# Optimization experiments

Measured on AMD Instinct MI355X. Metric: run time of the kernel, lower is better.

Reference implementation:

```python
import jax, jax.numpy as jnp
import numpy as np

N_NODES = 50000
N_EDGES = 800000
D_FEAT = 128
HIDDEN = 128
N_CLASSES = 40


def setup_inputs() -> dict:
    key = jax.random.key(0)
    ks = jax.random.split(key, 8)
    s = 1.0 / np.sqrt(D_FEAT)
    return {
        "x": jax.random.normal(ks[0], (N_NODES, D_FEAT), jnp.float32),
        "edge_index": jax.random.randint(ks[1], (2, N_EDGES), 0, N_NODES, jnp.int64),
        "Wl0": jax.random.normal(ks[2], (D_FEAT, HIDDEN), jnp.float32) * s,
        "bl0": jnp.zeros((HIDDEN,), jnp.float32),
        "Wr0": jax.random.normal(ks[3], (D_FEAT, HIDDEN), jnp.float32) * s,
        "Wl1": jax.random.normal(ks[4], (HIDDEN, HIDDEN), jnp.float32) * s,
        "bl1": jnp.zeros((HIDDEN,), jnp.float32),
        "Wr1": jax.random.normal(ks[5], (HIDDEN, HIDDEN), jnp.float32) * s,
        "Wl2": jax.random.normal(ks[6], (HIDDEN, N_CLASSES), jnp.float32) * s,
        "bl2": jnp.zeros((N_CLASSES,), jnp.float32),
        "Wr2": jax.random.normal(ks[7], (HIDDEN, N_CLASSES), jnp.float32) * s,
    }


def _sage_conv(x, src, dst, Wl, bl, Wr):
    # PyG SAGEConv (mean aggr): out = lin_l(mean_{j in N(i)} x_j) + lin_r(x_i)
    msg_sum = jax.ops.segment_sum(x[src], dst, num_segments=N_NODES)  # [N, d]
    deg = jax.ops.segment_sum(jnp.ones((src.shape[0],), x.dtype), dst, num_segments=N_NODES)
    mean = msg_sum / jnp.clip(deg, 1.0)[:, None]
    return mean @ Wl + bl + x @ Wr


def reference(x, edge_index, Wl0, bl0, Wr0, Wl1, bl1, Wr1, Wl2, bl2, Wr2):
    src, dst = edge_index[0], edge_index[1]
    h = jax.nn.relu(_sage_conv(x, src, dst, Wl0, bl0, Wr0))
    h = jax.nn.relu(_sage_conv(h, src, dst, Wl1, bl1, Wr1))
    h = jax.nn.relu(_sage_conv(h, src, dst, Wl2, bl2, Wr2))
    # dropout is identity in eval mode
    return jax.nn.log_softmax(h, axis=1)
```

## Files before the change

### kernel.cpp

```cpp
#include <hip/hip_runtime.h>
#include <cstdint>
#include <cstddef>
#include <cmath>

#define N_NODES 50000
#define N_EDGES 800000
#define D_FEAT 128
#define HIDDEN 128
#define N_CLASSES 40

typedef _Float16 half8 __attribute__((ext_vector_type(8)));
typedef _Float16 half4 __attribute__((ext_vector_type(4)));
typedef float f32x4 __attribute__((ext_vector_type(4)));


__global__ __launch_bounds__(256) void k_deg(const int* __restrict__ dst, int* __restrict__ deg,
                                             unsigned short* __restrict__ rank) {
    int e = blockIdx.x * 256 + threadIdx.x;
    if (e < N_EDGES) {
        int r = atomicAdd(&deg[dst[e]], 1);
        rank[e] = (unsigned short)r;
    }
}

__global__ __launch_bounds__(1024) void k_scan1(const int* __restrict__ deg, int* __restrict__ offsets,
                                                int* __restrict__ partials) {
    __shared__ int wsums[16];
    int tid = threadIdx.x;
    int g = blockIdx.x * 1024 + tid;
    int v = (g < N_NODES) ? deg[g] : 0;
    int lane = tid & 63;
    int wid = tid >> 6;
    int incl = v;
    #pragma unroll
    for (int off = 1; off < 64; off <<= 1) {
        int t = __shfl_up(incl, off);
        if (lane >= off) incl += t;
    }
    if (lane == 63) wsums[wid] = incl;
    __syncthreads();
    if (wid == 0) {
        int wv = (lane < 16) ? wsums[lane] : 0;
        int wincl = wv;
        #pragma unroll
        for (int off = 1; off < 16; off <<= 1) {
            int t = __shfl_up(wincl, off);
            if (lane >= off) wincl += t;
        }
        if (lane < 16) wsums[lane] = wincl - wv;
    }
    __syncthreads();
    if (g < N_NODES) offsets[g] = wsums[wid] + incl - v;
    if (tid == 1023) partials[blockIdx.x] = wsums[15] + incl;
}

__global__ __launch_bounds__(64) void k_scan2(int* __restrict__ partials, int nParts) {
    int lane = threadIdx.x;
    int v = (lane < nParts) ? partials[lane] : 0;
    int incl = v;
    #pragma unroll
    for (int off = 1; off < 64; off <<= 1) {
        int t = __shfl_up(incl, off);
        if (lane >= off) incl += t;
    }
    if (lane < nParts) partials[lane] = incl - v;
}

__global__ __launch_bounds__(256) void k_scan3(int* __restrict__ offsets, const int* __restrict__ partials) {
    int g = blockIdx.x * 256 + threadIdx.x;
    if (g < N_NODES) offsets[g] += partials[g >> 10];
}

__global__ __launch_bounds__(256) void k_scatter(const int* __restrict__ src, const int* __restrict__ dst,
                                                 const int* __restrict__ offsets,
                                                 const unsigned short* __restrict__ rank,
                                                 unsigned short* __restrict__ sorted_src) {
    int e = blockIdx.x * 256 + threadIdx.x;
    if (e < N_EDGES) {
        int d = dst[e];
        int pos = offsets[d] + (int)rank[e];
        sorted_src[pos] = (unsigned short)src[e];
    }
}


__global__ __launch_bounds__(256) void k_cvt(const float* __restrict__ in, _Float16* __restrict__ out, int n4) {
    int i = blockIdx.x * 256 + threadIdx.x;
    if (i < n4) {
        float4 v = *(const float4*)(in + (size_t)i * 4);
        half4 o;
        o[0] = (_Float16)v.x; o[1] = (_Float16)v.y; o[2] = (_Float16)v.z; o[3] = (_Float16)v.w;
        *(half4*)(out + (size_t)i * 4) = o;
    }
}


__global__ __launch_bounds__(64) void k_cvt_w(const float* __restrict__ Wl, const float* __restrict__ Wr,
                                              int Nout, int NF, _Float16* __restrict__ dst) {
    int t = blockIdx.x / NF;
    int f = blockIdx.x % NF;
    int l = threadIdx.x;
    int kb = t * 32 + (l >> 4) * 8;
    int n = f * 16 + (l & 15);
    half8 v;
    #pragma unroll
    for (int i = 0; i < 8; ++i) {
        int k = kb + i;
        float w = 0.f;
        if (n < Nout) w = (k < 128) ? Wl[k * Nout + n] : Wr[(k - 128) * Nout + n];
        v[i] = (_Float16)w;
    }
    *(half8*)(dst + ((size_t)(t * NF + f) * 64 + l) * 8) = v;
}


__global__ __launch_bounds__(256) void k_agg_h(const _Float16* __restrict__ feat, const int* __restrict__ offsets,
                                               const int* __restrict__ deg,
                                               const unsigned short* __restrict__ sorted_src,
                                               _Float16* __restrict__ mean) {
    int wave = (int)((blockIdx.x * 256 + threadIdx.x) >> 6);
    int lane = threadIdx.x & 63;
    if (wave >= N_NODES) return;
    int start = offsets[wave];
    int cnt = deg[wave];
    int grp = lane >> 4;
    int cl = lane & 15;
    float acc[8] = {0.f, 0.f, 0.f, 0.f, 0.f, 0.f, 0.f, 0.f};
    #pragma unroll 4
    for (int i = 0; i < cnt; i += 4) {
        int e = i + grp;
        if (e < cnt) {
            int s = (int)sorted_src[start + e];
            half8 v = *(const half8*)(feat + (size_t)s * 128 + cl * 8);
            #pragma unroll
            for (int j = 0; j < 8; ++j) acc[j] += (float)v[j];
        }
    }
    #pragma unroll
    for (int j = 0; j < 8; ++j) {
        acc[j] += __shfl_xor(acc[j], 16);
        acc[j] += __shfl_xor(acc[j], 32);
    }
    if (grp == 0) {
        float r = 1.0f / (float)(cnt > 0 ? cnt : 1);
        half8 o;
        #pragma unroll
        for (int j = 0; j < 8; ++j) o[j] = (_Float16)(acc[j] * r);
        *(half8*)(mean + (size_t)wave * 128 + cl * 8) = o;
    }
}


__global__ __launch_bounds__(256) void k_gemm_h(const _Float16* __restrict__ A, const _Float16* __restrict__ B,
                                                const _Float16* __restrict__ Wc, const float* __restrict__ bias,
                                                _Float16* __restrict__ outp) {
    int wv = (int)((blockIdx.x * 256 + threadIdx.x) >> 6);
    int rows0 = wv * 32;
    if (rows0 >= N_NODES) return;
    int lane = threadIdx.x & 63;
    int ln = lane & 15, lg = lane >> 4;
    int m0 = rows0 + ln;
    int m1 = m0 + 16;
    int m0c = m0 < N_NODES ? m0 : N_NODES - 1;
    int m1c = m1 < N_NODES ? m1 : N_NODES - 1;
    int klane = lg * 8;
    f32x4 acc[2][8];
    #pragma unroll
    for (int i = 0; i < 2; ++i)
        #pragma unroll
        for (int f = 0; f < 8; ++f) acc[i][f] = (f32x4){0.f, 0.f, 0.f, 0.f};
    #pragma unroll
    for (int t = 0; t < 8; ++t) {
        const _Float16* P = (t < 4) ? A : B;
        int koff = (t & 3) * 32 + klane;
        half8 a0 = *(const half8*)(P + (size_t)m0c * 128 + koff);
        half8 a1 = *(const half8*)(P + (size_t)m1c * 128 + koff);
        #pragma unroll
        for (int f = 0; f < 8; ++f) {
            half8 b = *(const half8*)(Wc + ((size_t)(t * 8 + f) * 64 + lane) * 8);
            acc[0][f] = __builtin_amdgcn_mfma_f32_16x16x32_f16(a0, b, acc[0][f], 0, 0, 0);
            acc[1][f] = __builtin_amdgcn_mfma_f32_16x16x32_f16(a1, b, acc[1][f], 0, 0, 0);
        }
    }
    #pragma unroll
    for (int mf = 0; mf < 2; ++mf) {
        #pragma unroll
        for (int f = 0; f < 8; ++f) {
            int n = f * 16 + ln;
            float bv = bias[n];
            #pragma unroll
            for (int r = 0; r < 4; ++r) {
                int m = rows0 + mf * 16 + lg * 4 + r;
                if (m < N_NODES) {
                    float v = fmaxf(acc[mf][f][r] + bv, 0.f);
                    outp[(size_t)m * 128 + n] = (_Float16)v;
                }
            }
        }
    }
}


__global__ __launch_bounds__(256) void k_gemm_f(const _Float16* __restrict__ A, const _Float16* __restrict__ B,
                                                const _Float16* __restrict__ Wc, const float* __restrict__ bias,
                                                float* __restrict__ outp) {
    int wv = (int)((blockIdx.x * 256 + threadIdx.x) >> 6);
    int rows0 = wv * 32;
    if (rows0 >= N_NODES) return;
    int lane = threadIdx.x & 63;
    int ln = lane & 15, lg = lane >> 4;
    int m0 = rows0 + ln;
    int m1 = m0 + 16;
    int m0c = m0 < N_NODES ? m0 : N_NODES - 1;
    int m1c = m1 < N_NODES ? m1 : N_NODES - 1;
    int klane = lg * 8;
    f32x4 acc[2][3];
    #pragma unroll
    for (int i = 0; i < 2; ++i)
        #pragma unroll
        for (int f = 0; f < 3; ++f) acc[i][f] = (f32x4){0.f, 0.f, 0.f, 0.f};
    #pragma unroll
    for (int t = 0; t < 8; ++t) {
        const _Float16* P = (t < 4) ? A : B;
        int koff = (t & 3) * 32 + klane;
        half8 a0 = *(const half8*)(P + (size_t)m0c * 128 + koff);
        half8 a1 = *(const half8*)(P + (size_t)m1c * 128 + koff);
        #pragma unroll
        for (int f = 0; f < 3; ++f) {
            half8 b = *(const half8*)(Wc + ((size_t)(t * 3 + f) * 64 + lane) * 8);
            acc[0][f] = __builtin_amdgcn_mfma_f32_16x16x32_f16(a0, b, acc[0][f], 0, 0, 0);
            acc[1][f] = __builtin_amdgcn_mfma_f32_16x16x32_f16(a1, b, acc[1][f], 0, 0, 0);
        }
    }
    float bv[3];
    #pragma unroll
    for (int f = 0; f < 3; ++f) {
        int n = f * 16 + ln;
        bv[f] = (n < N_CLASSES) ? bias[n] : 0.f;
    }
    #pragma unroll
    for (int mf = 0; mf < 2; ++mf) {
        #pragma unroll
        for (int r = 0; r < 4; ++r) {
            int m = rows0 + mf * 16 + lg * 4 + r;
            float v[3];
            float vmax = -INFINITY;
            #pragma unroll
            for (int f = 0; f < 3; ++f) {
                int n = f * 16 + ln;
                v[f] = fmaxf(acc[mf][f][r] + bv[f], 0.f);
                if (n < N_CLASSES) vmax = fmaxf(vmax, v[f]);
            }
            #pragma unroll
            for (int off = 1; off < 16; off <<= 1) vmax = fmaxf(vmax, __shfl_xor(vmax, off));
            float s = 0.f;
            #pragma unroll
            for (int f = 0; f < 3; ++f) {
                int n = f * 16 + ln;
                if (n < N_CLASSES) s += expf(v[f] - vmax);
            }
            #pragma unroll
            for (int off = 1; off < 16; off <<= 1) s += __shfl_xor(s, off);
            float lse = vmax + logf(s);
            if (m < N_NODES) {
                #pragma unroll
                for (int f = 0; f < 3; ++f) {
                    int n = f * 16 + ln;
                    if (n < N_CLASSES) outp[(size_t)m * N_CLASSES + n] = v[f] - lse;
                }
            }
        }
    }
}

extern "C" void kernel_launch(void* const* d_in, const int* in_sizes, int n_in,
                              void* d_out, int out_size, void* d_ws, size_t ws_size,
                              hipStream_t stream) {
    const float* x   = (const float*)d_in[0];
    const int*   ei  = (const int*)d_in[1];
    const float* Wl0 = (const float*)d_in[2];
    const float* bl0 = (const float*)d_in[3];
    const float* Wr0 = (const float*)d_in[4];
    const float* Wl1 = (const float*)d_in[5];
    const float* bl1 = (const float*)d_in[6];
    const float* Wr1 = (const float*)d_in[7];
    const float* Wl2 = (const float*)d_in[8];
    const float* bl2 = (const float*)d_in[9];
    const float* Wr2 = (const float*)d_in[10];
    float* out = (float*)d_out;

    const int* src = ei;
    const int* dst = ei + N_EDGES;

    int* offsets  = (int*)d_ws;
    int* deg      = offsets + 50016;
    int* partials = deg + 50016;
    unsigned short* rank   = (unsigned short*)(partials + 64);
    unsigned short* sorted = rank + N_EDGES;
    _Float16* xh  = (_Float16*)(sorted + N_EDGES);
    _Float16* mh  = xh + (size_t)N_NODES * 128;
    _Float16* h0  = mh + (size_t)N_NODES * 128;
    _Float16* h1  = h0 + (size_t)N_NODES * 128;
    _Float16* Wc0 = h1 + (size_t)N_NODES * 128;
    _Float16* Wc1 = Wc0 + 8 * 8 * 64 * 8;
    _Float16* Wc2 = Wc1 + 8 * 8 * 64 * 8;

    hipMemsetAsync(deg, 0, 50016 * sizeof(int), stream);

    const int edgeBlocks = (N_EDGES + 255) / 256;
    const int scanBlocks = (N_NODES + 1023) / 1024;
    k_deg<<<edgeBlocks, 256, 0, stream>>>(dst, deg, rank);
    k_scan1<<<scanBlocks, 1024, 0, stream>>>(deg, offsets, partials);
    k_scan2<<<1, 64, 0, stream>>>(partials, scanBlocks);
    k_scan3<<<(N_NODES + 255) / 256, 256, 0, stream>>>(offsets, partials);
    k_scatter<<<edgeBlocks, 256, 0, stream>>>(src, dst, offsets, rank, sorted);

    k_cvt<<<(N_NODES * 128 / 4 + 255) / 256, 256, 0, stream>>>(x, xh, N_NODES * 128 / 4);
    k_cvt_w<<<8 * 8, 64, 0, stream>>>(Wl0, Wr0, HIDDEN, 8, Wc0);
    k_cvt_w<<<8 * 8, 64, 0, stream>>>(Wl1, Wr1, HIDDEN, 8, Wc1);
    k_cvt_w<<<8 * 3, 64, 0, stream>>>(Wl2, Wr2, N_CLASSES, 3, Wc2);

    const int waveBlocks = (N_NODES * 64 + 255) / 256;
    const int gemmBlocks = ((N_NODES + 31) / 32 + 3) / 4;

    k_agg_h<<<waveBlocks, 256, 0, stream>>>(xh, offsets, deg, sorted, mh);
    k_gemm_h<<<gemmBlocks, 256, 0, stream>>>(mh, xh, Wc0, bl0, h0);
    k_agg_h<<<waveBlocks, 256, 0, stream>>>(h0, offsets, deg, sorted, mh);
    k_gemm_h<<<gemmBlocks, 256, 0, stream>>>(mh, h0, Wc1, bl1, h1);
    k_agg_h<<<waveBlocks, 256, 0, stream>>>(h1, offsets, deg, sorted, mh);
    k_gemm_f<<<gemmBlocks, 256, 0, stream>>>(mh, h1, Wc2, bl2, out);
}
```

Measured before the change: 324.0 us.

## Stage GEMM A/B tiles in swizzled LDS and merge conversion kernels into one

The two GEMM kernels now cooperatively load a 128-row block of both input matrices into XOR-swizzled shared memory with coalesced 16-byte loads. MFMA operands are then read from LDS instead of issuing strided per-lane global loads. The x conversion and the three weight-packing kernels are merged into a single launch to cut launch overhead. The cost is 64KB of LDS per block, which limits occupancy, plus an added barrier before compute.

```diff
diff --git a/kernel.cpp b/kernel.cpp
--- a/kernel.cpp
+++ b/kernel.cpp
@@ -84,22 +84,30 @@
 }
 
 
-__global__ __launch_bounds__(256) void k_cvt(const float* __restrict__ in, _Float16* __restrict__ out, int n4) {
-    int i = blockIdx.x * 256 + threadIdx.x;
-    if (i < n4) {
-        float4 v = *(const float4*)(in + (size_t)i * 4);
+#define CVT_BLOCKS 6250
+
+__global__ __launch_bounds__(256) void k_prep(const float* __restrict__ x, _Float16* __restrict__ xh,
+                                              const float* __restrict__ Wl0, const float* __restrict__ Wr0, _Float16* __restrict__ Wc0,
+                                              const float* __restrict__ Wl1, const float* __restrict__ Wr1, _Float16* __restrict__ Wc1,
+                                              const float* __restrict__ Wl2, const float* __restrict__ Wr2, _Float16* __restrict__ Wc2) {
+    int bid = blockIdx.x;
+    if (bid < CVT_BLOCKS) {
+        int i = bid * 256 + threadIdx.x;
+        float4 v = *(const float4*)(x + (size_t)i * 4);
         half4 o;
         o[0] = (_Float16)v.x; o[1] = (_Float16)v.y; o[2] = (_Float16)v.z; o[3] = (_Float16)v.w;
-        *(half4*)(out + (size_t)i * 4) = o;
-    }
-}
-
-
-__global__ __launch_bounds__(64) void k_cvt_w(const float* __restrict__ Wl, const float* __restrict__ Wr,
-                                              int Nout, int NF, _Float16* __restrict__ dst) {
-    int t = blockIdx.x / NF;
-    int f = blockIdx.x % NF;
-    int l = threadIdx.x;
+        *(half4*)(xh + (size_t)i * 4) = o;
+        return;
+    }
+    bid -= CVT_BLOCKS;
+    const float* Wl; const float* Wr; _Float16* dst; int NF, Nout, cell0;
+    if (bid < 16)      { Wl = Wl0; Wr = Wr0; dst = Wc0; NF = 8; Nout = 128; cell0 = bid * 4; }
+    else if (bid < 32) { Wl = Wl1; Wr = Wr1; dst = Wc1; NF = 8; Nout = 128; cell0 = (bid - 16) * 4; }
+    else               { Wl = Wl2; Wr = Wr2; dst = Wc2; NF = 3; Nout = 40;  cell0 = (bid - 32) * 4; }
+    int cell = cell0 + (threadIdx.x >> 6);
+    int t = cell / NF;
+    int f = cell % NF;
+    int l = threadIdx.x & 63;
     int kb = t * 32 + (l >> 4) * 8;
     int n = f * 16 + (l & 15);
     half8 v;
@@ -110,7 +118,7 @@
         if (n < Nout) w = (k < 128) ? Wl[k * Nout + n] : Wr[(k - 128) * Nout + n];
         v[i] = (_Float16)w;
     }
-    *(half8*)(dst + ((size_t)(t * NF + f) * 64 + l) * 8) = v;
+    *(half8*)(dst + ((size_t)cell * 64 + l) * 8) = v;
 }
 
 
@@ -154,16 +162,28 @@
 __global__ __launch_bounds__(256) void k_gemm_h(const _Float16* __restrict__ A, const _Float16* __restrict__ B,
                                                 const _Float16* __restrict__ Wc, const float* __restrict__ bias,
                                                 _Float16* __restrict__ outp) {
-    int wv = (int)((blockIdx.x * 256 + threadIdx.x) >> 6);
-    int rows0 = wv * 32;
-    if (rows0 >= N_NODES) return;
-    int lane = threadIdx.x & 63;
+    __shared__ _Float16 sA[128 * 128];
+    __shared__ _Float16 sB[128 * 128];
+    int tid = threadIdx.x;
+    int rows0 = blockIdx.x * 128;
+    for (int i = 0; i < 8; ++i) {
+        int cid = i * 256 + tid;
+        int r = cid >> 4;
+        int ch = cid & 15;
+        int gr = rows0 + r;
+        int grc = gr < N_NODES ? gr : N_NODES - 1;
+        half8 va = *(const half8*)(A + (size_t)grc * 128 + ch * 8);
+        half8 vb = *(const half8*)(B + (size_t)grc * 128 + ch * 8);
+        int sch = ch ^ (r & 15);
+        *(half8*)(sA + r * 128 + sch * 8) = va;
+        *(half8*)(sB + r * 128 + sch * 8) = vb;
+    }
+    __syncthreads();
+    int w = tid >> 6;
+    int lane = tid & 63;
     int ln = lane & 15, lg = lane >> 4;
-    int m0 = rows0 + ln;
-    int m1 = m0 + 16;
-    int m0c = m0 < N_NODES ? m0 : N_NODES - 1;
-    int m1c = m1 < N_NODES ? m1 : N_NODES - 1;
-    int klane = lg * 8;
+    int r0 = w * 32 + ln;
+    int r1 = r0 + 16;
     f32x4 acc[2][8];
     #pragma unroll
     for (int i = 0; i < 2; ++i)
@@ -171,10 +191,10 @@
         for (int f = 0; f < 8; ++f) acc[i][f] = (f32x4){0.f, 0.f, 0.f, 0.f};
     #pragma unroll
     for (int t = 0; t < 8; ++t) {
-        const _Float16* P = (t < 4) ? A : B;
-        int koff = (t & 3) * 32 + klane;
-        half8 a0 = *(const half8*)(P + (size_t)m0c * 128 + koff);
-        half8 a1 = *(const half8*)(P + (size_t)m1c * 128 + koff);
+        const _Float16* P = (t < 4) ? sA : sB;
+        int ch = (t & 3) * 4 + lg;
+        half8 a0 = *(const half8*)(P + r0 * 128 + (ch ^ (r0 & 15)) * 8);
+        half8 a1 = *(const half8*)(P + r1 * 128 + (ch ^ (r1 & 15)) * 8);
         #pragma unroll
         for (int f = 0; f < 8; ++f) {
             half8 b = *(const half8*)(Wc + ((size_t)(t * 8 + f) * 64 + lane) * 8);
@@ -182,6 +202,7 @@
             acc[1][f] = __builtin_amdgcn_mfma_f32_16x16x32_f16(a1, b, acc[1][f], 0, 0, 0);
         }
     }
+    int rw = rows0 + w * 32;
     #pragma unroll
     for (int mf = 0; mf < 2; ++mf) {
         #pragma unroll
@@ -190,7 +211,7 @@
             float bv = bias[n];
             #pragma unroll
             for (int r = 0; r < 4; ++r) {
-                int m = rows0 + mf * 16 + lg * 4 + r;
+                int m = rw + mf * 16 + lg * 4 + r;
                 if (m < N_NODES) {
                     float v = fmaxf(acc[mf][f][r] + bv, 0.f);
                     outp[(size_t)m * 128 + n] = (_Float16)v;
@@ -204,16 +225,28 @@
 __global__ __launch_bounds__(256) void k_gemm_f(const _Float16* __restrict__ A, const _Float16* __restrict__ B,
                                                 const _Float16* __restrict__ Wc, const float* __restrict__ bias,
                                                 float* __restrict__ outp) {
-    int wv = (int)((blockIdx.x * 256 + threadIdx.x) >> 6);
-    int rows0 = wv * 32;
-    if (rows0 >= N_NODES) return;
-    int lane = threadIdx.x & 63;
+    __shared__ _Float16 sA[128 * 128];
+    __shared__ _Float16 sB[128 * 128];
+    int tid = threadIdx.x;
+    int rows0 = blockIdx.x * 128;
+    for (int i = 0; i < 8; ++i) {
+        int cid = i * 256 + tid;
+        int r = cid >> 4;
+        int ch = cid & 15;
+        int gr = rows0 + r;
+        int grc = gr < N_NODES ? gr : N_NODES - 1;
+        half8 va = *(const half8*)(A + (size_t)grc * 128 + ch * 8);
+        half8 vb = *(const half8*)(B + (size_t)grc * 128 + ch * 8);
+        int sch = ch ^ (r & 15);
+        *(half8*)(sA + r * 128 + sch * 8) = va;
+        *(half8*)(sB + r * 128 + sch * 8) = vb;
+    }
+    __syncthreads();
+    int w = tid >> 6;
+    int lane = tid & 63;
     int ln = lane & 15, lg = lane >> 4;
-    int m0 = rows0 + ln;
-    int m1 = m0 + 16;
-    int m0c = m0 < N_NODES ? m0 : N_NODES - 1;
-    int m1c = m1 < N_NODES ? m1 : N_NODES - 1;
-    int klane = lg * 8;
+    int r0 = w * 32 + ln;
+    int r1 = r0 + 16;
     f32x4 acc[2][3];
     #pragma unroll
     for (int i = 0; i < 2; ++i)
@@ -221,10 +254,10 @@
         for (int f = 0; f < 3; ++f) acc[i][f] = (f32x4){0.f, 0.f, 0.f, 0.f};
     #pragma unroll
     for (int t = 0; t < 8; ++t) {
-        const _Float16* P = (t < 4) ? A : B;
-        int koff = (t & 3) * 32 + klane;
-        half8 a0 = *(const half8*)(P + (size_t)m0c * 128 + koff);
-        half8 a1 = *(const half8*)(P + (size_t)m1c * 128 + koff);
+        const _Float16* P = (t < 4) ? sA : sB;
+        int ch = (t & 3) * 4 + lg;
+        half8 a0 = *(const half8*)(P + r0 * 128 + (ch ^ (r0 & 15)) * 8);
+        half8 a1 = *(const half8*)(P + r1 * 128 + (ch ^ (r1 & 15)) * 8);
         #pragma unroll
         for (int f = 0; f < 3; ++f) {
             half8 b = *(const half8*)(Wc + ((size_t)(t * 3 + f) * 64 + lane) * 8);
@@ -238,11 +271,12 @@
         int n = f * 16 + ln;
         bv[f] = (n < N_CLASSES) ? bias[n] : 0.f;
     }
+    int rw = rows0 + w * 32;
     #pragma unroll
     for (int mf = 0; mf < 2; ++mf) {
         #pragma unroll
         for (int r = 0; r < 4; ++r) {
-            int m = rows0 + mf * 16 + lg * 4 + r;
+            int m = rw + mf * 16 + lg * 4 + r;
             float v[3];
             float vmax = -INFINITY;
             #pragma unroll
@@ -315,13 +349,10 @@
     k_scan3<<<(N_NODES + 255) / 256, 256, 0, stream>>>(offsets, partials);
     k_scatter<<<edgeBlocks, 256, 0, stream>>>(src, dst, offsets, rank, sorted);
 
-    k_cvt<<<(N_NODES * 128 / 4 + 255) / 256, 256, 0, stream>>>(x, xh, N_NODES * 128 / 4);
-    k_cvt_w<<<8 * 8, 64, 0, stream>>>(Wl0, Wr0, HIDDEN, 8, Wc0);
-    k_cvt_w<<<8 * 8, 64, 0, stream>>>(Wl1, Wr1, HIDDEN, 8, Wc1);
-    k_cvt_w<<<8 * 3, 64, 0, stream>>>(Wl2, Wr2, N_CLASSES, 3, Wc2);
+    k_prep<<<CVT_BLOCKS + 38, 256, 0, stream>>>(x, xh, Wl0, Wr0, Wc0, Wl1, Wr1, Wc1, Wl2, Wr2, Wc2);
 
     const int waveBlocks = (N_NODES * 64 + 255) / 256;
-    const int gemmBlocks = ((N_NODES + 31) / 32 + 3) / 4;
+    const int gemmBlocks = (N_NODES + 127) / 128;
 
     k_agg_h<<<waveBlocks, 256, 0, stream>>>(xh, offsets, deg, sorted, mh);
     k_gemm_h<<<gemmBlocks, 256, 0, stream>>>(mh, xh, Wc0, bl0, h0);
```

Measured after the change: 309.8 us. 1.05x faster.
